# Performance work log

Measured on AMD Instinct MI355X. Metric: run time of the kernel, lower is better.

Reference implementation:

```python
import jax, jax.numpy as jnp
import numpy as np

B, N, D, H = 2, 2048, 1024, 16
HD = D // H
SCALE = HD ** -0.5


def setup_inputs() -> dict:
    key = jax.random.key(0)
    ks = jax.random.split(key, 5)
    s = D ** -0.5  # keep activations well-scaled like torch Linear init
    return {
        "x": jax.random.normal(ks[0], (B, N, D), jnp.float32),
        "Wq": jax.random.normal(ks[1], (D, D), jnp.float32) * s,
        "bq": jnp.zeros((D,), jnp.float32),
        "Wk": jax.random.normal(ks[2], (D, D), jnp.float32) * s,
        "bk": jnp.zeros((D,), jnp.float32),
        "Wv": jax.random.normal(ks[3], (D, D), jnp.float32) * s,
        "bv": jnp.zeros((D,), jnp.float32),
        "Wo": jax.random.normal(ks[4], (D, D), jnp.float32) * s,
        "bo": jnp.zeros((D,), jnp.float32),
    }


def reference(x, Wq, bq, Wk, bk, Wv, bv, Wo, bo):
    # projections: [B,N,D] -> [B,H,N,HD]
    def split_heads(t):
        return t.reshape(B, N, H, HD).transpose(0, 2, 1, 3)

    q = split_heads(x @ Wq + bq)
    k = split_heads(x @ Wk + bk)
    v = split_heads(x @ Wv + bv)
    # eager attention: explicit [B,H,N,N] scores, matching the torch module
    attn = jnp.einsum("bhnd,bhmd->bhnm", q, k) * SCALE
    attn = jax.nn.softmax(attn, axis=-1)
    out = jnp.einsum("bhnm,bhmd->bhnd", attn, v)
    out = out.transpose(0, 2, 1, 3).reshape(B, N, D)
    return out @ Wo + bo
```

## Files before the change

### kernel.cpp

```cpp
#include <hip/hip_runtime.h>
#include <hip/hip_bf16.h>

typedef __attribute__((ext_vector_type(8))) short bf16x8;
typedef __attribute__((ext_vector_type(4))) float f32x4;
typedef __attribute__((ext_vector_type(4))) unsigned short us4;
typedef __attribute__((ext_vector_type(8))) unsigned short us8;
typedef unsigned short u16;

#define NB 2
#define NSEQ 2048
#define DM 1024
#define NH 16
#define HD 64
#define NTOK (NB*NSEQ)
#define QK_SCALE (0.125f * 1.4426950408889634f)

__device__ __forceinline__ u16 f2b(float f) {
  __hip_bfloat16 h = __float2bfloat16(f);
  return __builtin_bit_cast(u16, h);
}

__device__ __forceinline__ unsigned pkbf(float a, float b) {
  return (unsigned)f2b(a) | ((unsigned)f2b(b) << 16);
}

__device__ __forceinline__ void gload16(const void* g, void* l) {
  __builtin_amdgcn_global_load_lds((__attribute__((address_space(1))) void*)g,
                                   (__attribute__((address_space(3))) void*)l, 16, 0, 0);
}

__global__ __launch_bounds__(256) void k_convx(const float* __restrict__ x, u16* __restrict__ xb) {
  const int idx = (blockIdx.x * 256 + threadIdx.x) * 8;
  const float4 v0 = *(const float4*)(x + idx);
  const float4 v1 = *(const float4*)(x + idx + 4);
  us8 o;
  o[0]=f2b(v0.x); o[1]=f2b(v0.y); o[2]=f2b(v0.z); o[3]=f2b(v0.w);
  o[4]=f2b(v1.x); o[5]=f2b(v1.y); o[6]=f2b(v1.z); o[7]=f2b(v1.w);
  *(us8*)(xb + idx) = o;
}

__global__ __launch_bounds__(256) void k_twt4(const float* __restrict__ W0, const float* __restrict__ W1,
                                              const float* __restrict__ W2, const float* __restrict__ W3,
                                              u16* __restrict__ T0, u16* __restrict__ T1,
                                              u16* __restrict__ T2, u16* __restrict__ T3) {
  const float* W = (blockIdx.z == 0) ? W0 : (blockIdx.z == 1) ? W1 : (blockIdx.z == 2) ? W2 : W3;
  u16* WT = (blockIdx.z == 0) ? T0 : (blockIdx.z == 1) ? T1 : (blockIdx.z == 2) ? T2 : T3;
  __shared__ float tile[64][68];
  const int n0 = blockIdx.x * 64, k0 = blockIdx.y * 64;
  const int tr = threadIdx.x >> 4, tc = (threadIdx.x & 15) * 4;
#pragma unroll
  for (int rr = 0; rr < 4; ++rr) {
    const int r = rr * 16 + tr;
    *(float4*)&tile[r][tc] = *(const float4*)&W[(size_t)(k0 + r) * DM + n0 + tc];
  }
  __syncthreads();
#pragma unroll
  for (int rr = 0; rr < 4; ++rr) {
    const int nr = rr * 16 + tr;
    us4 o;
#pragma unroll
    for (int e = 0; e < 4; ++e) o[e] = f2b(tile[tc + e][nr]);
    *(us4*)&WT[(size_t)(n0 + nr) * DM + k0 + tc] = o;
  }
}

__global__ __launch_bounds__(256) void k_gemm_qkv(
    const u16* __restrict__ xb,
    const u16* __restrict__ WqT, const u16* __restrict__ WkT, const u16* __restrict__ WvT,
    const float* __restrict__ bq, const float* __restrict__ bk, const float* __restrict__ bv,
    u16* __restrict__ Qb, u16* __restrict__ Kb, u16* __restrict__ Vtb)
{
  const int z = blockIdx.z;
  const bool isV = (z == 2);
  const u16* Ap = (z == 0) ? WqT : (z == 1) ? WkT : xb;
  const u16* Bt = isV ? WvT : xb;
  const float* bp = (z == 0) ? bq : (z == 1) ? bk : bv;
  const float scale = (z == 0) ? QK_SCALE : 1.0f;
  u16* outp = (z == 0) ? Qb : (z == 1) ? Kb : Vtb;
  const int i0 = isV ? blockIdx.x * 128 : blockIdx.y * 128;
  const int j0 = isV ? blockIdx.y * 128 : blockIdx.x * 128;

  __shared__ char smem[64 * 1024];
  const int tid = threadIdx.x, lane = tid & 63, wv = tid >> 6;
  const int li = lane & 15, g = lane >> 4;
  const int wi = wv >> 1, wj = wv & 1;

  f32x4 acc[4][4];
#pragma unroll
  for (int a = 0; a < 4; ++a)
#pragma unroll
    for (int b = 0; b < 4; ++b) acc[a][b] = f32x4{0.f, 0.f, 0.f, 0.f};

  auto stage = [&](int kt, int buf) {
#pragma unroll
    for (int c = 0; c < 4; ++c) {
      const int lg = c * 256 + tid;
      const int r = lg >> 3, ch = (lg & 7) ^ (r & 7);
      gload16(Ap + (size_t)(i0 + r) * 1024 + kt * 64 + ch * 8,
              smem + buf * 32768 + (c * 256 + wv * 64) * 16);
      gload16(Bt + (size_t)(j0 + r) * 1024 + kt * 64 + ch * 8,
              smem + buf * 32768 + 16384 + (c * 256 + wv * 64) * 16);
    }
  };

  stage(0, 0);

  for (int kt = 0; kt < 16; ++kt) {
    __syncthreads();
    if (kt + 1 < 16) stage(kt + 1, (kt + 1) & 1);
    const char* As = smem + (kt & 1) * 32768;
    const char* Bs = As + 16384;
#pragma unroll
    for (int ks = 0; ks < 2; ++ks) {
      bf16x8 af[4], bfr[4];
#pragma unroll
      for (int it = 0; it < 4; ++it) {
        const int ri = 64 * wi + 16 * it + li;
        af[it] = *(const bf16x8*)(As + ri * 128 + ((ks * 64 + g * 16) ^ ((ri & 7) << 4)));
        const int rj = 64 * wj + 16 * it + li;
        bfr[it] = *(const bf16x8*)(Bs + rj * 128 + ((ks * 64 + g * 16) ^ ((rj & 7) << 4)));
      }
#pragma unroll
      for (int it = 0; it < 4; ++it)
#pragma unroll
        for (int jt = 0; jt < 4; ++jt)
          acc[it][jt] = __builtin_amdgcn_mfma_f32_16x16x32_bf16(af[it], bfr[jt], acc[it][jt], 0, 0, 0);
    }
  }

#pragma unroll
  for (int it = 0; it < 4; ++it) {
    const int ib = i0 + 64 * wi + 16 * it + 4 * g;
    f32x4 b4;
    if (!isV) b4 = *(const f32x4*)(bp + ib);
#pragma unroll
    for (int jt = 0; jt < 4; ++jt) {
      const int j = j0 + 64 * wj + 16 * jt + li;
      f32x4 v = acc[it][jt];
      if (!isV) {
        v += b4;
        v *= scale;
        us4 pk; pk[0]=f2b(v[0]); pk[1]=f2b(v[1]); pk[2]=f2b(v[2]); pk[3]=f2b(v[3]);
        *(us4*)(outp + (size_t)j * 1024 + ib) = pk;
      } else {
        const float bj = bp[j];
        v[0] += bj; v[1] += bj; v[2] += bj; v[3] += bj;
        us4 pk; pk[0]=f2b(v[0]); pk[1]=f2b(v[1]); pk[2]=f2b(v[2]); pk[3]=f2b(v[3]);
        const size_t addr = ((size_t)(ib >> 11) * 1024 + j) * 2048 + (ib & 2047);
        *(us4*)(outp + addr) = pk;
      }
    }
  }
}

__global__ __launch_bounds__(256) void k_gemm_out(
    const u16* __restrict__ A, const u16* __restrict__ Bt, const float* __restrict__ bias,
    float* __restrict__ outp)
{
  __shared__ char smem[64 * 1024];
  const int tid = threadIdx.x, lane = tid & 63, wv = tid >> 6;
  const int li = lane & 15, g = lane >> 4;
  const int wi = wv >> 1, wj = wv & 1;
  const int i0 = blockIdx.y * 128, j0 = blockIdx.x * 128;

  f32x4 acc[4][4];
#pragma unroll
  for (int a = 0; a < 4; ++a)
#pragma unroll
    for (int b = 0; b < 4; ++b) acc[a][b] = f32x4{0.f, 0.f, 0.f, 0.f};

  auto stage = [&](int kt, int buf) {
#pragma unroll
    for (int c = 0; c < 4; ++c) {
      const int lg = c * 256 + tid;
      const int r = lg >> 3, ch = (lg & 7) ^ (r & 7);
      gload16(A + (size_t)(i0 + r) * 1024 + kt * 64 + ch * 8,
              smem + buf * 32768 + (c * 256 + wv * 64) * 16);
      gload16(Bt + (size_t)(j0 + r) * 1024 + kt * 64 + ch * 8,
              smem + buf * 32768 + 16384 + (c * 256 + wv * 64) * 16);
    }
  };

  stage(0, 0);

  for (int kt = 0; kt < 16; ++kt) {
    __syncthreads();
    if (kt + 1 < 16) stage(kt + 1, (kt + 1) & 1);
    const char* As = smem + (kt & 1) * 32768;
    const char* Bs = As + 16384;
#pragma unroll
    for (int ks = 0; ks < 2; ++ks) {
      bf16x8 af[4], bfr[4];
#pragma unroll
      for (int it = 0; it < 4; ++it) {
        const int ri = 64 * wi + 16 * it + li;
        af[it] = *(const bf16x8*)(As + ri * 128 + ((ks * 64 + g * 16) ^ ((ri & 7) << 4)));
        const int rj = 64 * wj + 16 * it + li;
        bfr[it] = *(const bf16x8*)(Bs + rj * 128 + ((ks * 64 + g * 16) ^ ((rj & 7) << 4)));
      }
#pragma unroll
      for (int it = 0; it < 4; ++it)
#pragma unroll
        for (int jt = 0; jt < 4; ++jt)
          acc[it][jt] = __builtin_amdgcn_mfma_f32_16x16x32_bf16(af[it], bfr[jt], acc[it][jt], 0, 0, 0);
    }
  }

#pragma unroll
  for (int it = 0; it < 4; ++it) {
    const int ib = i0 + 64 * wi + 16 * it + 4 * g;
    const f32x4 b4 = *(const f32x4*)(bias + ib);
#pragma unroll
    for (int jt = 0; jt < 4; ++jt) {
      const int j = j0 + 64 * wj + 16 * jt + li;
      f32x4 v = acc[it][jt] + b4;
      *(f32x4*)(outp + (size_t)j * 1024 + ib) = v;
    }
  }
}

__global__ __launch_bounds__(256, 2) void k_attn(const u16* __restrict__ Q, const u16* __restrict__ K,
                                                 const u16* __restrict__ Vt, u16* __restrict__ O)
{
  __shared__ char smem[48 * 1024];
  const int tid = threadIdx.x, lane = tid & 63, w = tid >> 6;
  const int li = lane & 15, g = lane >> 4;

  const int vid = blockIdx.x;
  const int u = vid >> 3;
  const int bh = (vid & 7) * 4 + (u >> 4);
  const int qt = u & 15;
  const int b = bh >> 4, h = bh & 15;
  const int n0 = qt * 128;
  const size_t tokbase = (size_t)b * NSEQ;
  const int iq = 16 * w + li;

  bf16x8 qf[2][2];
#pragma unroll
  for (int grp = 0; grp < 2; ++grp)
#pragma unroll
    for (int ks = 0; ks < 2; ++ks)
      qf[grp][ks] = *(const bf16x8*)(Q + (tokbase + n0 + 64 * grp + iq) * 1024 + h * 64 + 32 * ks + 8 * g);

  bf16x8 ones;
#pragma unroll
  for (int e = 0; e < 8; ++e) ones[e] = (short)0x3F80;

  f32x4 oacc[2][4];
#pragma unroll
  for (int grp = 0; grp < 2; ++grp)
#pragma unroll
    for (int dt = 0; dt < 4; ++dt) oacc[grp][dt] = f32x4{0.f, 0.f, 0.f, 0.f};
  f32x4 ls[2] = {f32x4{0.f,0.f,0.f,0.f}, f32x4{0.f,0.f,0.f,0.f}};

  const u16* Kb = K + tokbase * 1024 + h * 64;
  const u16* Vb = Vt + (size_t)bh * 64 * 2048;

  auto stage = [&](int t, int buf) {
    const int jn = t * 64;
#pragma unroll
    for (int c = 0; c < 2; ++c) {
      const int lg = c * 256 + tid;
      const int r = lg >> 3, ch = (lg & 7) ^ (r & 7);
      gload16(Kb + (size_t)(jn + r) * 1024 + ch * 8, smem + buf * 8192 + (c * 256 + w * 64) * 16);
      gload16(Vb + (size_t)r * 2048 + jn + ch * 8, smem + 16384 + buf * 8192 + (c * 256 + w * 64) * 16);
    }
  };

  auto tilebody = [&](int t, int buf) {
    __syncthreads();
    if (t + 1 < 32) stage(t + 1, buf ^ 1);
    const char* Ks = smem + buf * 8192;
    const char* Vs = smem + 16384 + buf * 8192;

    f32x4 s[2][4];
#pragma unroll
    for (int grp = 0; grp < 2; ++grp)
#pragma unroll
      for (int jt = 0; jt < 4; ++jt) s[grp][jt] = f32x4{0.f, 0.f, 0.f, 0.f};
#pragma unroll
    for (int ks = 0; ks < 2; ++ks) {
#pragma unroll
      for (int jt = 0; jt < 4; ++jt) {
        const int rj = 16 * jt + li;
        bf16x8 a = *(const bf16x8*)(Ks + rj * 128 + ((ks * 64 + g * 16) ^ ((rj & 7) << 4)));
        s[0][jt] = __builtin_amdgcn_mfma_f32_16x16x32_bf16(a, qf[0][ks], s[0][jt], 0, 0, 0);
        s[1][jt] = __builtin_amdgcn_mfma_f32_16x16x32_bf16(a, qf[1][ks], s[1][jt], 0, 0, 0);
      }
    }

#pragma unroll
    for (int grp = 0; grp < 2; ++grp) {
      const int row = iq + 64 * grp;
      char* Pr = smem + 32768 + row * 128;
      const int swz = (row & 7) << 4;
#pragma unroll
      for (int jt = 0; jt < 4; ++jt) {
        uint2 pk;
        pk.x = pkbf(exp2f(s[grp][jt][0]), exp2f(s[grp][jt][1]));
        pk.y = pkbf(exp2f(s[grp][jt][2]), exp2f(s[grp][jt][3]));
        *(uint2*)(Pr + ((32 * jt + 8 * g) ^ swz)) = pk;
      }
    }

#pragma unroll
    for (int ks = 0; ks < 2; ++ks) {
      const int kb = ks * 64 + g * 16;
      bf16x8 bpv0 = *(const bf16x8*)(smem + 32768 + iq * 128 + (kb ^ ((iq & 7) << 4)));
      bf16x8 bpv1 = *(const bf16x8*)(smem + 32768 + (iq + 64) * 128 + (kb ^ ((iq & 7) << 4)));
      ls[0] = __builtin_amdgcn_mfma_f32_16x16x32_bf16(ones, bpv0, ls[0], 0, 0, 0);
      ls[1] = __builtin_amdgcn_mfma_f32_16x16x32_bf16(ones, bpv1, ls[1], 0, 0, 0);
#pragma unroll
      for (int dt = 0; dt < 4; ++dt) {
        const int rd = 16 * dt + li;
        bf16x8 av = *(const bf16x8*)(Vs + rd * 128 + (kb ^ ((rd & 7) << 4)));
        oacc[0][dt] = __builtin_amdgcn_mfma_f32_16x16x32_bf16(av, bpv0, oacc[0][dt], 0, 0, 0);
        oacc[1][dt] = __builtin_amdgcn_mfma_f32_16x16x32_bf16(av, bpv1, oacc[1][dt], 0, 0, 0);
      }
    }
  };

  stage(0, 0);
#pragma unroll 1
  for (int tt = 0; tt < 16; ++tt) {
    tilebody(2 * tt, 0);
    tilebody(2 * tt + 1, 1);
  }

#pragma unroll
  for (int grp = 0; grp < 2; ++grp) {
    const float inv = 1.f / ls[grp][0];
    const size_t obase = (tokbase + n0 + 64 * grp + iq) * 1024 + h * 64;
#pragma unroll
    for (int dt = 0; dt < 4; ++dt) {
      us4 pk;
#pragma unroll
      for (int e = 0; e < 4; ++e) pk[e] = f2b(oacc[grp][dt][e] * inv);
      *(us4*)(O + obase + 16 * dt + 4 * g) = pk;
    }
  }
}

extern "C" void kernel_launch(void* const* d_in, const int* in_sizes, int n_in,
                              void* d_out, int out_size, void* d_ws, size_t ws_size,
                              hipStream_t stream) {
  const float* x  = (const float*)d_in[0];
  const float* Wq = (const float*)d_in[1];
  const float* bq = (const float*)d_in[2];
  const float* Wk = (const float*)d_in[3];
  const float* bk = (const float*)d_in[4];
  const float* Wv = (const float*)d_in[5];
  const float* bv = (const float*)d_in[6];
  const float* Wo = (const float*)d_in[7];
  const float* bo = (const float*)d_in[8];

  char* ws = (char*)d_ws;
  u16* xb  = (u16*)(ws);
  u16* WqT = (u16*)(ws + (8  << 20));
  u16* WkT = (u16*)(ws + (10 << 20));
  u16* WvT = (u16*)(ws + (12 << 20));
  u16* WoT = (u16*)(ws + (14 << 20));
  u16* Qb  = (u16*)(ws + (16 << 20));
  u16* Kb  = (u16*)(ws + (24 << 20));
  u16* Vtb = (u16*)(ws + (32 << 20));
  u16* Ob  = (u16*)(ws + (40 << 20));

  k_convx<<<2048, 256, 0, stream>>>(x, xb);
  k_twt4<<<dim3(16, 16, 4), 256, 0, stream>>>(Wq, Wk, Wv, Wo, WqT, WkT, WvT, WoT);

  k_gemm_qkv<<<dim3(32, 8, 3), 256, 0, stream>>>(xb, WqT, WkT, WvT, bq, bk, bv, Qb, Kb, Vtb);

  k_attn<<<512, 256, 0, stream>>>(Qb, Kb, Vtb, Ob);

  k_gemm_out<<<dim3(32, 8), 256, 0, stream>>>(WoT, Ob, bo, (float*)d_out);
}
```

Before: 127.4 us.

## Shrink QKV k-tile, halve out-proj N tile, use packed bf16 convert in attention

The QKV GEMM now stages 32-wide k-slices in 32KB of LDS, with a 4-chunk swizzle over 32 k-steps, which should let more blocks reside per CU. The output GEMM tile becomes 128x64 with each wave owning 32 rows, doubling the grid to 512 blocks for better CU fill, at the cost of lower reuse per block. The attention softmax replaces two scalar bf16 conversions with the hardware v_cvt_pk_bf16_f32 instruction. The risks are more barriers per GEMM and more redundant A-operand loads.

```diff
diff --git a/kernel.cpp b/kernel.cpp
--- a/kernel.cpp
+++ b/kernel.cpp
@@ -20,8 +20,10 @@
   return __builtin_bit_cast(u16, h);
 }
 
-__device__ __forceinline__ unsigned pkbf(float a, float b) {
-  return (unsigned)f2b(a) | ((unsigned)f2b(b) << 16);
+__device__ __forceinline__ unsigned cvtpk(float a, float b) {
+  unsigned r;
+  asm("v_cvt_pk_bf16_f32 %0, %1, %2" : "=v"(r) : "v"(a), "v"(b));
+  return r;
 }
 
 __device__ __forceinline__ void gload16(const void* g, void* l) {
@@ -80,7 +82,7 @@
   const int i0 = isV ? blockIdx.x * 128 : blockIdx.y * 128;
   const int j0 = isV ? blockIdx.y * 128 : blockIdx.x * 128;
 
-  __shared__ char smem[64 * 1024];
+  __shared__ char smem[32 * 1024];
   const int tid = threadIdx.x, lane = tid & 63, wv = tid >> 6;
   const int li = lane & 15, g = lane >> 4;
   const int wi = wv >> 1, wj = wv & 1;
@@ -93,39 +95,36 @@
 
   auto stage = [&](int kt, int buf) {
 #pragma unroll
-    for (int c = 0; c < 4; ++c) {
+    for (int c = 0; c < 2; ++c) {
       const int lg = c * 256 + tid;
-      const int r = lg >> 3, ch = (lg & 7) ^ (r & 7);
-      gload16(Ap + (size_t)(i0 + r) * 1024 + kt * 64 + ch * 8,
-              smem + buf * 32768 + (c * 256 + wv * 64) * 16);
-      gload16(Bt + (size_t)(j0 + r) * 1024 + kt * 64 + ch * 8,
-              smem + buf * 32768 + 16384 + (c * 256 + wv * 64) * 16);
+      const int r = lg >> 2, ch = (lg & 3) ^ (r & 3);
+      gload16(Ap + (size_t)(i0 + r) * 1024 + kt * 32 + ch * 8,
+              smem + buf * 16384 + lg * 16);
+      gload16(Bt + (size_t)(j0 + r) * 1024 + kt * 32 + ch * 8,
+              smem + buf * 16384 + 8192 + lg * 16);
     }
   };
 
   stage(0, 0);
 
-  for (int kt = 0; kt < 16; ++kt) {
+  for (int kt = 0; kt < 32; ++kt) {
     __syncthreads();
-    if (kt + 1 < 16) stage(kt + 1, (kt + 1) & 1);
-    const char* As = smem + (kt & 1) * 32768;
-    const char* Bs = As + 16384;
-#pragma unroll
-    for (int ks = 0; ks < 2; ++ks) {
-      bf16x8 af[4], bfr[4];
-#pragma unroll
-      for (int it = 0; it < 4; ++it) {
-        const int ri = 64 * wi + 16 * it + li;
-        af[it] = *(const bf16x8*)(As + ri * 128 + ((ks * 64 + g * 16) ^ ((ri & 7) << 4)));
-        const int rj = 64 * wj + 16 * it + li;
-        bfr[it] = *(const bf16x8*)(Bs + rj * 128 + ((ks * 64 + g * 16) ^ ((rj & 7) << 4)));
-      }
-#pragma unroll
-      for (int it = 0; it < 4; ++it)
-#pragma unroll
-        for (int jt = 0; jt < 4; ++jt)
-          acc[it][jt] = __builtin_amdgcn_mfma_f32_16x16x32_bf16(af[it], bfr[jt], acc[it][jt], 0, 0, 0);
-    }
+    if (kt + 1 < 32) stage(kt + 1, (kt + 1) & 1);
+    const char* As = smem + (kt & 1) * 16384;
+    const char* Bs = As + 8192;
+    bf16x8 af[4], bfr[4];
+#pragma unroll
+    for (int it = 0; it < 4; ++it) {
+      const int ri = 64 * wi + 16 * it + li;
+      af[it] = *(const bf16x8*)(As + ri * 64 + ((g * 16) ^ ((ri & 3) << 4)));
+      const int rj = 64 * wj + 16 * it + li;
+      bfr[it] = *(const bf16x8*)(Bs + rj * 64 + ((g * 16) ^ ((rj & 3) << 4)));
+    }
+#pragma unroll
+    for (int it = 0; it < 4; ++it)
+#pragma unroll
+      for (int jt = 0; jt < 4; ++jt)
+        acc[it][jt] = __builtin_amdgcn_mfma_f32_16x16x32_bf16(af[it], bfr[jt], acc[it][jt], 0, 0, 0);
   }
 
 #pragma unroll
@@ -157,15 +156,14 @@
     const u16* __restrict__ A, const u16* __restrict__ Bt, const float* __restrict__ bias,
     float* __restrict__ outp)
 {
-  __shared__ char smem[64 * 1024];
+  __shared__ char smem[48 * 1024];
   const int tid = threadIdx.x, lane = tid & 63, wv = tid >> 6;
   const int li = lane & 15, g = lane >> 4;
-  const int wi = wv >> 1, wj = wv & 1;
-  const int i0 = blockIdx.y * 128, j0 = blockIdx.x * 128;
-
-  f32x4 acc[4][4];
-#pragma unroll
-  for (int a = 0; a < 4; ++a)
+  const int i0 = blockIdx.y * 128, j0 = blockIdx.x * 64;
+
+  f32x4 acc[2][4];
+#pragma unroll
+  for (int a = 0; a < 2; ++a)
 #pragma unroll
     for (int b = 0; b < 4; ++b) acc[a][b] = f32x4{0.f, 0.f, 0.f, 0.f};
 
@@ -175,9 +173,14 @@
       const int lg = c * 256 + tid;
       const int r = lg >> 3, ch = (lg & 7) ^ (r & 7);
       gload16(A + (size_t)(i0 + r) * 1024 + kt * 64 + ch * 8,
-              smem + buf * 32768 + (c * 256 + wv * 64) * 16);
+              smem + buf * 24576 + lg * 16);
+    }
+#pragma unroll
+    for (int c = 0; c < 2; ++c) {
+      const int lg = c * 256 + tid;
+      const int r = lg >> 3, ch = (lg & 7) ^ (r & 7);
       gload16(Bt + (size_t)(j0 + r) * 1024 + kt * 64 + ch * 8,
-              smem + buf * 32768 + 16384 + (c * 256 + wv * 64) * 16);
+              smem + buf * 24576 + 16384 + lg * 16);
     }
   };
 
@@ -186,20 +189,23 @@
   for (int kt = 0; kt < 16; ++kt) {
     __syncthreads();
     if (kt + 1 < 16) stage(kt + 1, (kt + 1) & 1);
-    const char* As = smem + (kt & 1) * 32768;
+    const char* As = smem + (kt & 1) * 24576;
     const char* Bs = As + 16384;
 #pragma unroll
     for (int ks = 0; ks < 2; ++ks) {
-      bf16x8 af[4], bfr[4];
-#pragma unroll
-      for (int it = 0; it < 4; ++it) {
-        const int ri = 64 * wi + 16 * it + li;
+      bf16x8 af[2], bfr[4];
+#pragma unroll
+      for (int it = 0; it < 2; ++it) {
+        const int ri = 32 * wv + 16 * it + li;
         af[it] = *(const bf16x8*)(As + ri * 128 + ((ks * 64 + g * 16) ^ ((ri & 7) << 4)));
-        const int rj = 64 * wj + 16 * it + li;
-        bfr[it] = *(const bf16x8*)(Bs + rj * 128 + ((ks * 64 + g * 16) ^ ((rj & 7) << 4)));
-      }
-#pragma unroll
-      for (int it = 0; it < 4; ++it)
+      }
+#pragma unroll
+      for (int jt = 0; jt < 4; ++jt) {
+        const int rj = 16 * jt + li;
+        bfr[jt] = *(const bf16x8*)(Bs + rj * 128 + ((ks * 64 + g * 16) ^ ((rj & 7) << 4)));
+      }
+#pragma unroll
+      for (int it = 0; it < 2; ++it)
 #pragma unroll
         for (int jt = 0; jt < 4; ++jt)
           acc[it][jt] = __builtin_amdgcn_mfma_f32_16x16x32_bf16(af[it], bfr[jt], acc[it][jt], 0, 0, 0);
@@ -207,12 +213,12 @@
   }
 
 #pragma unroll
-  for (int it = 0; it < 4; ++it) {
-    const int ib = i0 + 64 * wi + 16 * it + 4 * g;
+  for (int it = 0; it < 2; ++it) {
+    const int ib = i0 + 32 * wv + 16 * it + 4 * g;
     const f32x4 b4 = *(const f32x4*)(bias + ib);
 #pragma unroll
     for (int jt = 0; jt < 4; ++jt) {
-      const int j = j0 + 64 * wj + 16 * jt + li;
+      const int j = j0 + 16 * jt + li;
       f32x4 v = acc[it][jt] + b4;
       *(f32x4*)(outp + (size_t)j * 1024 + ib) = v;
     }
@@ -297,8 +303,8 @@
 #pragma unroll
       for (int jt = 0; jt < 4; ++jt) {
         uint2 pk;
-        pk.x = pkbf(exp2f(s[grp][jt][0]), exp2f(s[grp][jt][1]));
-        pk.y = pkbf(exp2f(s[grp][jt][2]), exp2f(s[grp][jt][3]));
+        pk.x = cvtpk(exp2f(s[grp][jt][0]), exp2f(s[grp][jt][1]));
+        pk.y = cvtpk(exp2f(s[grp][jt][2]), exp2f(s[grp][jt][3]));
         *(uint2*)(Pr + ((32 * jt + 8 * g) ^ swz)) = pk;
       }
     }
@@ -372,5 +378,5 @@
 
   k_attn<<<512, 256, 0, stream>>>(Qb, Kb, Vtb, Ob);
 
-  k_gemm_out<<<dim3(32, 8), 256, 0, stream>>>(WoT, Ob, bo, (float*)d_out);
-}
+  k_gemm_out<<<dim3(64, 8), 256, 0, stream>>>(WoT, Ob, bo, (float*)d_out);
+}
```

Measured after the change: 123.0 us. -3.5%, faster.
